# Kernel optimization log

Hardware: AMD Instinct MI355X
Metric: run time of the kernel (lower is better)

Reference implementation:

```python
import jax, jax.numpy as jnp
import numpy as np

N = 40000        # num nodes
E = 640000       # num edges
F_IN = 512
F_OUT = 32
HEADS = 8
NEG_SLOPE = 0.2
EPS = 1e-16


def setup_inputs() -> dict:
    key = jax.random.key(0)
    k1, k2, k3, k4, k5 = jax.random.split(key, 5)
    x = jax.random.normal(k1, (N, F_IN), dtype=jnp.float32)
    edge_index = jax.random.randint(k2, (2, E), 0, N, dtype=jnp.int32)
    # xavier-uniform-like init scales
    lim_W = float(np.sqrt(6.0 / (F_IN + F_OUT)))
    lim_a = float(np.sqrt(6.0 / (HEADS + F_OUT)))
    W = jax.random.uniform(k3, (HEADS, F_IN, F_OUT), dtype=jnp.float32, minval=-lim_W, maxval=lim_W)
    a_src = jax.random.uniform(k4, (HEADS, F_OUT), dtype=jnp.float32, minval=-lim_a, maxval=lim_a)
    a_dst = jax.random.uniform(k5, (HEADS, F_OUT), dtype=jnp.float32, minval=-lim_a, maxval=lim_a)
    bias = jnp.zeros((HEADS * F_OUT,), dtype=jnp.float32)
    return {"x": x, "edge_index": edge_index, "W": W, "a_src": a_src, "a_dst": a_dst, "bias": bias}


def reference(x, edge_index, W, a_src, a_dst, bias):
    src, dst = edge_index[0], edge_index[1]
    # per-head projection: [N, H, F_out]
    h = jnp.einsum('nd,hdf->nhf', x, W)
    # attention logit pieces computed per-node then gathered per-edge
    # (same math as gathering h then dotting with a)
    s_src = jnp.einsum('nhf,hf->nh', h, a_src)   # [N, H]
    s_dst = jnp.einsum('nhf,hf->nh', h, a_dst)   # [N, H]
    e = s_src[src] + s_dst[dst]                  # [E, H]
    e = jnp.where(e >= 0, e, NEG_SLOPE * e)      # LeakyReLU(0.2)
    # edge softmax over incoming edges of each dst node (global max shift, as in source)
    e = e - jnp.max(e)
    exp_e = jnp.exp(e)
    denom = jax.ops.segment_sum(exp_e, dst, num_segments=N)   # [N, H]
    alpha = exp_e / (denom[dst] + EPS)                        # [E, H]
    # weighted message aggregation (dropout is identity in eval / p=0)
    msg = alpha[..., None] * h[src]                           # [E, H, F_out]
    out = jax.ops.segment_sum(msg, dst, num_segments=N)       # [N, H, F_out]
    out = out.reshape(N, HEADS * F_OUT) + bias                # concat=True
    return out
```

## Files before the change

### kernel.cpp

```cpp
#include <hip/hip_runtime.h>
#include <hip/hip_bf16.h>
#include <math.h>
#include <stdint.h>

#define N_NODES 40000
#define N_EDGES 640000
#define F_IN    512
#define F_OUT   32
#define HEADS   8
#define C_OUT   (HEADS * F_OUT)
#define NEG_SLOPE 0.2f
#define EPS_F   1e-16f
#define MAXDEG  64

typedef __attribute__((ext_vector_type(8)))  short  short8;
typedef __attribute__((ext_vector_type(4)))  short  short4v;
typedef __attribute__((ext_vector_type(16))) float  float16v;

__device__ __forceinline__ void splitT(float f, unsigned short& hi, unsigned short& lo) {
    unsigned u = __float_as_uint(f);
    hi = (unsigned short)(u >> 16);
    float r = f - __uint_as_float(u & 0xFFFF0000u);
    lo = (unsigned short)(__float_as_uint(r) >> 16);
}

__device__ __forceinline__ unsigned short f2bf(float f) {
    unsigned u = __float_as_uint(f);
    return (unsigned short)((u + 0x7FFF + ((u >> 16) & 1)) >> 16);
}

#define BARRIER_NOVM() asm volatile("s_waitcnt lgkmcnt(0)\n\ts_barrier" ::: "memory")

__global__ __launch_bounds__(256) void pack_zero(const float* __restrict__ W,
                                                 unsigned short* __restrict__ Bp,
                                                 int* __restrict__ cursor) {
    if (blockIdx.x < 512) {
        int tid = blockIdx.x * 256 + threadIdx.x;
        int j    = tid & 7;
        int L    = (tid >> 3) & 63;
        int ni   = (tid >> 9) & 1;
        int ktg  = (tid >> 10) & 31;
        int wc   = tid >> 15;
        int k    = ktg * 16 + (L >> 5) * 8 + j;
        int col  = wc * 64 + ni * 32 + (L & 31);
        int hh = col >> 5, f = col & 31;
        Bp[tid] = f2bf(W[hh * (F_IN * F_OUT) + k * F_OUT + f]);
    } else {
        int i = (blockIdx.x - 512) * 256 + threadIdx.x;
        if (i < N_NODES / 4)
            *(int4*)&cursor[i * 4] = (int4){0, 0, 0, 0};
    }
}

#define AS 66
#define GEMM_BLOCKS 1250
#define SCAT_BLOCKS 1250

__global__ __launch_bounds__(512, 4) void gemm_scatter(const float* __restrict__ x,
                                                       const unsigned short* __restrict__ Bp,
                                                       const float* __restrict__ a_src,
                                                       const float* __restrict__ a_dst,
                                                       unsigned short* __restrict__ h16,
                                                       float* __restrict__ s_src,
                                                       float* __restrict__ s_dst,
                                                       const int* __restrict__ src,
                                                       const int* __restrict__ dst,
                                                       int* __restrict__ cursor,
                                                       int* __restrict__ src_buf) {
    if (blockIdx.x >= GEMM_BLOCKS) {
        int e = (blockIdx.x - GEMM_BLOCKS) * 512 + threadIdx.x;
        int s = src[e], d = dst[e];
        int pos = atomicAdd(&cursor[d], 1);
        if (pos < MAXDEG) src_buf[d * MAXDEG + pos] = s;
        return;
    }

    __shared__ unsigned short As_hi[2][32 * AS];
    __shared__ unsigned short As_lo[2][32 * AS];

    const int t = threadIdx.x;
    const int wc = t >> 6, L = t & 63;
    const int r31 = L & 31, half = L >> 5;
    const int n0 = blockIdx.x * 32;

    float16v accH, accL;
#pragma unroll
    for (int r = 0; r < 16; ++r) { accH[r] = 0.f; accL[r] = 0.f; }

    const int kcol = (t & 15) * 4;
    const int rbase = t >> 4;
    const float* xp = &x[(size_t)(n0 + rbase) * F_IN + kcol];

    const unsigned short* bp =
        &Bp[((((size_t)(wc >> 1) * 32) * 2 + (wc & 1)) * 64 + L) * 8];

#define CONVW(b, s0) do {                                                      \
        unsigned short h0,h1,h2,h3,l0,l1,l2,l3;                                \
        splitT((s0).x,h0,l0); splitT((s0).y,h1,l1);                            \
        splitT((s0).z,h2,l2); splitT((s0).w,h3,l3);                            \
        int off_ = rbase*AS + kcol;                                            \
        *(short4v*)&As_hi[b][off_] =                                           \
            (short4v){(short)h0,(short)h1,(short)h2,(short)h3};                \
        *(short4v*)&As_lo[b][off_] =                                           \
            (short4v){(short)l0,(short)l1,(short)l2,(short)l3};                \
    } while (0)

    float4 stgA = *(const float4*)(xp);
    float4 stgB = *(const float4*)(xp + 64);
    CONVW(0, stgA);
    BARRIER_NOVM();

#pragma unroll
    for (int st = 0; st < 8; ++st) {
        const int cur = st & 1, nxt = cur ^ 1;

        short8 breg[4];
#pragma unroll
        for (int kt = 0; kt < 4; ++kt)
            breg[kt] = *(const short8*)(bp + (size_t)(st * 4 + kt) * 1024);

        float4 stgC = stgB;
        if (st < 6) stgC = *(const float4*)(xp + (st + 2) * 64);

        if (st < 7) CONVW(nxt, stgB);

#pragma unroll
        for (int kt = 0; kt < 4; ++kt) {
            int off = r31 * AS + kt * 16 + half * 8;
            short8 ah = *(const short8*)&As_hi[cur][off];
            short8 al = *(const short8*)&As_lo[cur][off];
            accH = __builtin_amdgcn_mfma_f32_32x32x16_bf16(ah, breg[kt], accH, 0, 0, 0);
            accL = __builtin_amdgcn_mfma_f32_32x32x16_bf16(al, breg[kt], accL, 0, 0, 0);
        }

        if (st < 7) BARRIER_NOVM();
        stgB = stgC;
    }
#undef CONVW

#pragma unroll
    for (int r = 0; r < 16; ++r) accH[r] += accL[r];

    const int colb = wc * 32 + r31;
#pragma unroll
    for (int r = 0; r < 16; ++r) {
        int row = n0 + (r & 3) + 8 * (r >> 2) + 4 * half;
        h16[(size_t)row * C_OUT + colb] = f2bf(accH[r]);
    }

    {
        float af = a_src[wc * 32 + r31];
        float df = a_dst[wc * 32 + r31];
#pragma unroll
        for (int r = 0; r < 16; ++r) {
            float v = accH[r];
            float vs = v * af;
            float vd = v * df;
#pragma unroll
            for (int m = 1; m < 32; m <<= 1) {
                vs += __shfl_xor(vs, m, 64);
                vd += __shfl_xor(vd, m, 64);
            }
            if (r31 == 0) {
                int row = n0 + (r & 3) + 8 * (r >> 2) + 4 * half;
                s_src[row * 8 + wc] = vs;
                s_dst[row * 8 + wc] = vd;
            }
        }
    }
}

__global__ __launch_bounds__(256) void aggregate(const int* __restrict__ src_buf,
                                                 const unsigned short* __restrict__ h16,
                                                 const float* __restrict__ s_src,
                                                 const float* __restrict__ s_dst,
                                                 const int* __restrict__ cursor,
                                                 const float* __restrict__ bias,
                                                 float* __restrict__ out) {
    const int t = threadIdx.x;
    const int wave = t >> 6, lane = t & 63;
    const int wgid = blockIdx.x * 4 + wave;
    const int ch0 = lane * 4;
    const int hh = lane >> 3;
    const int eL = lane & 7;
    const int gbase = lane & 56;

    auto bf2f = [](short v) { return __uint_as_float(((unsigned)(unsigned short)v) << 16); };
    const float4 b4 = *(const float4*)&bias[ch0];

    for (int n = wgid; n < N_NODES; n += 8192) {
        const int start = n * MAXDEG;
        const int cnt = cursor[n];
        const float sd = s_dst[n * 8 + hh];

        float a0 = 0.f, a1 = 0.f, a2 = 0.f, a3 = 0.f, den = 0.f;

        int base = 0;
        for (; base + 8 <= cnt; base += 8) {
            int idx = start + base;
            int s[8];
#pragma unroll
            for (int u = 0; u < 8; ++u)
                s[u] = src_buf[idx + u];

            short4v v[8];
#pragma unroll
            for (int u = 0; u < 8; ++u)
                v[u] = *(const short4v*)&h16[(size_t)s[u] * C_OUT + ch0];

            float sc = s_src[s[eL] * 8 + hh] + sd;
            sc = sc >= 0.f ? sc : NEG_SLOPE * sc;
            float wx = __expf(sc);

            float w[8];
#pragma unroll
            for (int u = 0; u < 8; ++u)
                w[u] = __shfl(wx, gbase | u, 64);

#pragma unroll
            for (int u = 0; u < 8; ++u) {
                a0 += w[u] * bf2f(v[u][0]);
                a1 += w[u] * bf2f(v[u][1]);
                a2 += w[u] * bf2f(v[u][2]);
                a3 += w[u] * bf2f(v[u][3]);
                den += w[u];
            }
        }

        int rem = cnt - base;
        if (rem > 0) {
            int idx = start + base;
            int s[8];
#pragma unroll
            for (int u = 0; u < 8; ++u)
                s[u] = (u < rem) ? src_buf[idx + u] : 0;

            short4v v[8];
#pragma unroll
            for (int u = 0; u < 8; ++u)
                v[u] = *(const short4v*)&h16[(size_t)s[u] * C_OUT + ch0];

            float sc = s_src[s[eL] * 8 + hh] + sd;
            sc = sc >= 0.f ? sc : NEG_SLOPE * sc;
            float wx = __expf(sc);

            float w[8];
#pragma unroll
            for (int u = 0; u < 8; ++u) {
                float ws = __shfl(wx, gbase | u, 64);
                w[u] = (u < rem) ? ws : 0.f;
            }

#pragma unroll
            for (int u = 0; u < 8; ++u) {
                a0 += w[u] * bf2f(v[u][0]);
                a1 += w[u] * bf2f(v[u][1]);
                a2 += w[u] * bf2f(v[u][2]);
                a3 += w[u] * bf2f(v[u][3]);
                den += w[u];
            }
        }

        float inv = 1.0f / (den + EPS_F);
        float4 o;
        o.x = a0 * inv + b4.x;
        o.y = a1 * inv + b4.y;
        o.z = a2 * inv + b4.z;
        o.w = a3 * inv + b4.w;
        *(float4*)&out[(size_t)n * C_OUT + ch0] = o;
    }
}

extern "C" void kernel_launch(void* const* d_in, const int* in_sizes, int n_in,
                              void* d_out, int out_size, void* d_ws, size_t ws_size,
                              hipStream_t stream) {
    const float* x     = (const float*)d_in[0];
    const int*   eidx  = (const int*)d_in[1];
    const float* W     = (const float*)d_in[2];
    const float* a_src = (const float*)d_in[3];
    const float* a_dst = (const float*)d_in[4];
    const float* bias  = (const float*)d_in[5];
    float* out = (float*)d_out;

    const int* src = eidx;
    const int* dst = eidx + N_EDGES;

    char* p = (char*)d_ws;
    auto carve = [&](size_t bytes) {
        char* r = p;
        p += (bytes + 255) & ~(size_t)255;
        return r;
    };
    unsigned short* h16 = (unsigned short*)carve((size_t)N_NODES * C_OUT * 2);
    float* s_src      = (float*)carve((size_t)N_NODES * HEADS * 4);
    float* s_dst      = (float*)carve((size_t)N_NODES * HEADS * 4);
    int*   src_buf    = (int*)carve((size_t)N_NODES * MAXDEG * 4);
    int*   cursor     = (int*)carve((size_t)N_NODES * 4);
    unsigned short* Bp = (unsigned short*)carve((size_t)131072 * 2);

    pack_zero<<<552, 256, 0, stream>>>(W, Bp, cursor);
    gemm_scatter<<<GEMM_BLOCKS + SCAT_BLOCKS, 512, 0, stream>>>(
        x, Bp, a_src, a_dst, h16, s_src, s_dst, src, dst, cursor, src_buf);
    aggregate<<<2048, 256, 0, stream>>>(src_buf, h16, s_src, s_dst,
                                        cursor, bias, out);
}
```

Baseline: 242.1 us.

## Prefetch B fragments and deepen pipelining in projection and aggregation kernels

In the projection GEMM, B-operand registers for the next stage and the x staging loads for two stages ahead are now loaded early, so global load latency overlaps the MFMA work. In the aggregation kernel, each wave loads the node's full source-index list once into a register and distributes indices by shuffle. It double-buffers gathers of 8-edge batches so the next batch's h16 rows and s_src scores are in flight while the current batch is accumulated. It also prefetches the next node's metadata. This raises register pressure and may reduce occupancy.

```diff
diff --git a/kernel.cpp b/kernel.cpp
--- a/kernel.cpp
+++ b/kernel.cpp
@@ -106,7 +106,12 @@
     } while (0)
 
     float4 stgA = *(const float4*)(xp);
+    short8 breg[4];
+#pragma unroll
+    for (int kt = 0; kt < 4; ++kt)
+        breg[kt] = *(const short8*)(bp + (size_t)kt * 1024);
     float4 stgB = *(const float4*)(xp + 64);
+    float4 stgC = *(const float4*)(xp + 128);
     CONVW(0, stgA);
     BARRIER_NOVM();
 
@@ -114,13 +119,15 @@
     for (int st = 0; st < 8; ++st) {
         const int cur = st & 1, nxt = cur ^ 1;
 
-        short8 breg[4];
-#pragma unroll
-        for (int kt = 0; kt < 4; ++kt)
-            breg[kt] = *(const short8*)(bp + (size_t)(st * 4 + kt) * 1024);
-
-        float4 stgC = stgB;
-        if (st < 6) stgC = *(const float4*)(xp + (st + 2) * 64);
+        short8 bregN[4];
+        if (st < 7) {
+#pragma unroll
+            for (int kt = 0; kt < 4; ++kt)
+                bregN[kt] = *(const short8*)(bp + (size_t)((st + 1) * 4 + kt) * 1024);
+        }
+
+        float4 stgD = stgC;
+        if (st < 5) stgD = *(const float4*)(xp + (st + 3) * 64);
 
         if (st < 7) CONVW(nxt, stgB);
 
@@ -134,7 +141,10 @@
         }
 
         if (st < 7) BARRIER_NOVM();
-        stgB = stgC;
+
+        stgB = stgC; stgC = stgD;
+#pragma unroll
+        for (int kt = 0; kt < 4; ++kt) breg[kt] = bregN[kt];
     }
 #undef CONVW
 
@@ -188,78 +198,70 @@
     auto bf2f = [](short v) { return __uint_as_float(((unsigned)(unsigned short)v) << 16); };
     const float4 b4 = *(const float4*)&bias[ch0];
 
+    int sRegP = src_buf[wgid * MAXDEG + lane];
+    int cntP  = cursor[wgid];
+    float sdP = s_dst[wgid * 8 + hh];
+
     for (int n = wgid; n < N_NODES; n += 8192) {
-        const int start = n * MAXDEG;
-        const int cnt = cursor[n];
-        const float sd = s_dst[n * 8 + hh];
+        const int nn = n + 8192;
+        int sRegN = 0, cntN = 0; float sdN = 0.f;
+        if (nn < N_NODES) {
+            sRegN = src_buf[nn * MAXDEG + lane];
+            cntN  = cursor[nn];
+            sdN   = s_dst[nn * 8 + hh];
+        }
+
+        const int cnt = cntP;
+        const float sd = sdP;
+        const int sReg = (lane < cnt) ? sRegP : 0;
 
         float a0 = 0.f, a1 = 0.f, a2 = 0.f, a3 = 0.f, den = 0.f;
-
-        int base = 0;
-        for (; base + 8 <= cnt; base += 8) {
-            int idx = start + base;
-            int s[8];
-#pragma unroll
-            for (int u = 0; u < 8; ++u)
-                s[u] = src_buf[idx + u];
-
-            short4v v[8];
-#pragma unroll
-            for (int u = 0; u < 8; ++u)
-                v[u] = *(const short4v*)&h16[(size_t)s[u] * C_OUT + ch0];
-
-            float sc = s_src[s[eL] * 8 + hh] + sd;
-            sc = sc >= 0.f ? sc : NEG_SLOPE * sc;
-            float wx = __expf(sc);
-
-            float w[8];
-#pragma unroll
-            for (int u = 0; u < 8; ++u)
-                w[u] = __shfl(wx, gbase | u, 64);
-
-#pragma unroll
-            for (int u = 0; u < 8; ++u) {
-                a0 += w[u] * bf2f(v[u][0]);
-                a1 += w[u] * bf2f(v[u][1]);
-                a2 += w[u] * bf2f(v[u][2]);
-                a3 += w[u] * bf2f(v[u][3]);
-                den += w[u];
+        const int nb = (cnt + 7) >> 3;
+
+        short4v vA[8], vB[8];
+        float scA = 0.f, scB = 0.f;
+        int vldA = 0, vldB = 0;
+
+#define PREF_(V, SC, VLD, b) do {                                              \
+        _Pragma("unroll")                                                      \
+        for (int u = 0; u < 8; ++u) {                                          \
+            int id_ = __shfl(sReg, (b) * 8 + u, 64);                           \
+            V[u] = *(const short4v*)&h16[(size_t)id_ * C_OUT + ch0];           \
+        }                                                                      \
+        int own_ = __shfl(sReg, (b) * 8 + eL, 64);                             \
+        SC = s_src[own_ * 8 + hh];                                             \
+        VLD = ((b) * 8 + eL) < cnt;                                            \
+    } while (0)
+
+#define CONS_(V, SC, VLD) do {                                                 \
+        float e_ = SC + sd;                                                    \
+        e_ = e_ >= 0.f ? e_ : NEG_SLOPE * e_;                                  \
+        float wx_ = VLD ? __expf(e_) : 0.f;                                    \
+        _Pragma("unroll")                                                      \
+        for (int u = 0; u < 8; ++u) {                                          \
+            float w_ = __shfl(wx_, gbase | u, 64);                             \
+            a0 += w_ * bf2f(V[u][0]);                                          \
+            a1 += w_ * bf2f(V[u][1]);                                          \
+            a2 += w_ * bf2f(V[u][2]);                                          \
+            a3 += w_ * bf2f(V[u][3]);                                          \
+            den += w_;                                                         \
+        }                                                                      \
+    } while (0)
+
+        if (nb > 0) {
+            PREF_(vA, scA, vldA, 0);
+            int b = 0;
+            while (true) {
+                if (b + 1 < nb) PREF_(vB, scB, vldB, b + 1);
+                CONS_(vA, scA, vldA);
+                if (++b >= nb) break;
+                if (b + 1 < nb) PREF_(vA, scA, vldA, b + 1);
+                CONS_(vB, scB, vldB);
+                if (++b >= nb) break;
             }
         }
-
-        int rem = cnt - base;
-        if (rem > 0) {
-            int idx = start + base;
-            int s[8];
-#pragma unroll
-            for (int u = 0; u < 8; ++u)
-                s[u] = (u < rem) ? src_buf[idx + u] : 0;
-
-            short4v v[8];
-#pragma unroll
-            for (int u = 0; u < 8; ++u)
-                v[u] = *(const short4v*)&h16[(size_t)s[u] * C_OUT + ch0];
-
-            float sc = s_src[s[eL] * 8 + hh] + sd;
-            sc = sc >= 0.f ? sc : NEG_SLOPE * sc;
-            float wx = __expf(sc);
-
-            float w[8];
-#pragma unroll
-            for (int u = 0; u < 8; ++u) {
-                float ws = __shfl(wx, gbase | u, 64);
-                w[u] = (u < rem) ? ws : 0.f;
-            }
-
-#pragma unroll
-            for (int u = 0; u < 8; ++u) {
-                a0 += w[u] * bf2f(v[u][0]);
-                a1 += w[u] * bf2f(v[u][1]);
-                a2 += w[u] * bf2f(v[u][2]);
-                a3 += w[u] * bf2f(v[u][3]);
-                den += w[u];
-            }
-        }
+#undef PREF_
+#undef CONS_
 
         float inv = 1.0f / (den + EPS_F);
         float4 o;
@@ -268,6 +270,8 @@
         o.z = a2 * inv + b4.z;
         o.w = a3 * inv + b4.w;
         *(float4*)&out[(size_t)n * C_OUT + ch0] = o;
+
+        sRegP = sRegN; cntP = cntN; sdP = sdN;
     }
 }
 
```

New measurement: 248.2 us. 2.5% more time.
